# Kernel tuning notes

Measured on AMD Instinct MI355X. Metric: run time of the kernel, lower is better.

The kernel has to match this reference:

```python
import jax, jax.numpy as jnp
import numpy as np

NUM_EMBEDDINGS = 2048
EMBEDDING_DIM = 256
COMMITMENT_COST = 0.25


def setup_inputs() -> dict:
    key = jax.random.key(0)
    k1, k2 = jax.random.split(key)
    z_e = jax.random.normal(k1, (64, EMBEDDING_DIM, 32, 32), dtype=jnp.float32)
    # nn.Embedding weight initialized uniform(-1/K, 1/K)
    bound = 1.0 / NUM_EMBEDDINGS
    codebook = jax.random.uniform(k2, (NUM_EMBEDDINGS, EMBEDDING_DIM),
                                  dtype=jnp.float32, minval=-bound, maxval=bound)
    return {"z_e": z_e, "codebook": codebook}


def reference(z_e, codebook):
    B, C, H, W = z_e.shape  # C == embedding_dim
    K = codebook.shape[0]
    sg = jax.lax.stop_gradient

    # [B, C, H, W] -> [B*H*W, C]
    z_e_flat = jnp.transpose(z_e, (0, 2, 3, 1)).reshape(-1, C)

    # squared L2 distances: ||z||^2 - 2 z E^T + ||E||^2  -> [N, K]
    distances = (jnp.sum(z_e_flat ** 2, axis=1, keepdims=True)
                 - 2.0 * jnp.matmul(z_e_flat, codebook.T)
                 + jnp.sum(codebook ** 2, axis=1))
    indices = jnp.argmin(distances, axis=1)  # [N]

    encodings = jax.nn.one_hot(indices, K, dtype=z_e_flat.dtype)  # [N, K]
    z_q_flat = codebook[indices]  # [N, C] embedding gather
    z_q = jnp.transpose(z_q_flat.reshape(B, H, W, C), (0, 3, 1, 2))

    codebook_loss = jnp.mean((z_q_flat - sg(z_e_flat)) ** 2)
    commitment_loss = jnp.mean((sg(z_q_flat) - z_e_flat) ** 2)
    loss = codebook_loss + COMMITMENT_COST * commitment_loss

    e_mean = jnp.mean(encodings, axis=0)  # [K]
    perplexity = jnp.exp(-jnp.sum(e_mean * jnp.log(e_mean + 1e-10)))

    # straight-through estimator
    z_q_st = z_e + sg(z_q - z_e)
    return z_q_st, loss, perplexity, encodings
```

## Files before the change

### kernel.cpp

```cpp
#include <hip/hip_runtime.h>
#include <hip/hip_bf16.h>
#include <math.h>

#define NTOT 65536
#define KCB  2048
#define CDIM 256
#define HW   1024

#define OUT_LOSS 16777216
#define OUT_PERP 16777217
#define OUT_ENC  16777218

#define CBB_OFF_F 33554448

#define WS_CK   262144
#define WS_IDX  270336
#define WS_CNT  532480
#define WS_PART 540672

#define MARGIN 3e-3f
#define CAP 1024

typedef __attribute__((ext_vector_type(8))) short short8;
typedef __attribute__((ext_vector_type(4))) float f32x4;

__device__ inline unsigned enc_f(float x) {
    unsigned u = __float_as_uint(x);
    return (u & 0x80000000u) ? ~u : (u | 0x80000000u);
}
__device__ inline float dec_f(unsigned e) {
    unsigned u = (e & 0x80000000u) ? (e ^ 0x80000000u) : ~e;
    return __uint_as_float(u);
}

__device__ inline void lds_min_u64(unsigned long long* p, unsigned long long v) {
    unsigned long long old = *p;
    while (v < old) {
        unsigned long long assumed = old;
        old = atomicCAS(p, assumed, v);
        if (old == assumed) break;
    }
}

__global__ __launch_bounds__(256) void k_prep_cb(const float* __restrict__ cb, ushort* __restrict__ cbb,
                                                 float* __restrict__ ck, int* __restrict__ cntK) {
    const int tid = threadIdx.x;
    const int wv = tid >> 6, lane = tid & 63;
    const int r = blockIdx.x * 4 + wv;
    const float* row = cb + (size_t)r * CDIM;
    float4 v = *(const float4*)(row + lane * 4);
    ushort4 o;
    __hip_bfloat16 h;
    h = __float2bfloat16(v.x); o.x = *(ushort*)&h;
    h = __float2bfloat16(v.y); o.y = *(ushort*)&h;
    h = __float2bfloat16(v.z); o.z = *(ushort*)&h;
    h = __float2bfloat16(v.w); o.w = *(ushort*)&h;
    *(ushort4*)(cbb + (size_t)r * CDIM + lane * 4) = o;
    float s = v.x*v.x + v.y*v.y + v.z*v.z + v.w*v.w;
    for (int off = 32; off >= 1; off >>= 1) s += __shfl_down(s, off, 64);
    if (lane == 0) ck[r] = s;
    if (lane == 1) cntK[r] = 0;
}

__global__ __launch_bounds__(256, 2) void k_main(
    const float* __restrict__ z, const float* __restrict__ cb,
    const ushort* __restrict__ cbb, const float* __restrict__ ckg,
    int* __restrict__ indices, int* __restrict__ cntK,
    float* __restrict__ out0, double* __restrict__ part)
{
    __shared__ float ztb[CDIM * 65];
    __shared__ union {
        struct {
            unsigned long long wmin[4][64];
            float thrRow[64];
            float srowL[64];
            int   candRK[CAP];
        } p1;
        float  qc[32 * 65];
        double sh[256];
    } u;
    __shared__ unsigned long long best[64];
    __shared__ int cnt;
    __shared__ int allscan;

    const int tid = threadIdx.x;
    const int w = tid >> 6, lane = tid & 63;
    const int col = lane & 15, quad = lane >> 4;
    const int n0 = blockIdx.x * 64;
    const int b = n0 >> 10, hw0 = n0 & 1023;

    {
        const int hwq = tid & 15, csub = (tid >> 4) & 3;
#pragma unroll
        for (int i = 0; i < 16; ++i) {
            const int c = w * 64 + i * 4 + csub;
            float4 v = *(const float4*)(z + ((size_t)b * CDIM + c) * HW + hw0 + hwq * 4);
            float* dst = ztb + c * 65 + hwq * 4;
            dst[0] = v.x; dst[1] = v.y; dst[2] = v.z; dst[3] = v.w;
        }
    }
    if (tid == 0) { cnt = 0; allscan = 0; }
    __syncthreads();

    short8 areg[4][8];
#pragma unroll
    for (int nt = 0; nt < 4; ++nt)
#pragma unroll
        for (int cs = 0; cs < 8; ++cs) {
            short8 a;
#pragma unroll
            for (int j = 0; j < 8; ++j) {
                __hip_bfloat16 h = __float2bfloat16(ztb[(cs * 32 + quad * 8 + j) * 65 + nt * 16 + col]);
                a[j] = *(ushort*)&h;
            }
            areg[nt][cs] = a;
        }

    if (tid < 64) {
        float s = 0.f;
#pragma unroll 8
        for (int c = 0; c < CDIM; ++c) { float v = ztb[c * 65 + tid]; s = fmaf(v, v, s); }
        u.p1.srowL[tid] = s;
    }

    float m1[16], m2[16]; int k1[16];
#pragma unroll
    for (int s = 0; s < 16; ++s) { m1[s] = INFINITY; m2[s] = INFINITY; k1[s] = 0; }

    for (int k0 = 0; k0 < KCB; k0 += 128) {
        const int kb = k0 + w * 32;
#pragma unroll
        for (int kt = 0; kt < 2; ++kt) {
            const int kk = kb + kt * 16 + col;
            const ushort* bbase = cbb + (size_t)kk * CDIM + quad * 8;
            short8 bfrag[8];
#pragma unroll
            for (int cs = 0; cs < 8; ++cs) bfrag[cs] = *(const short8*)(bbase + cs * 32);
            f32x4 acc[4];
#pragma unroll
            for (int nt = 0; nt < 4; ++nt) acc[nt] = (f32x4){0.f, 0.f, 0.f, 0.f};
#pragma unroll
            for (int cs = 0; cs < 8; ++cs)
#pragma unroll
                for (int nt = 0; nt < 4; ++nt)
                    acc[nt] = __builtin_amdgcn_mfma_f32_16x16x32_bf16(areg[nt][cs], bfrag[cs], acc[nt], 0, 0, 0);
            const float ckv = ckg[kk];
#pragma unroll
            for (int nt = 0; nt < 4; ++nt)
#pragma unroll
                for (int r = 0; r < 4; ++r) {
                    float dt = fmaf(-2.0f, acc[nt][r], ckv);
                    const int s = nt * 4 + r;
                    bool c = dt < m1[s];
                    m2[s] = fminf(m2[s], fmaxf(dt, m1[s]));
                    m1[s] = fminf(m1[s], dt);
                    k1[s] = c ? kk : k1[s];
                }
        }
    }

#pragma unroll
    for (int s = 0; s < 16; ++s) {
        unsigned long long v = ((unsigned long long)enc_f(m1[s]) << 32) | (unsigned)k1[s];
#pragma unroll
        for (int m = 1; m <= 8; m <<= 1) {
            unsigned long long o = __shfl_xor(v, m, 64);
            v = (o < v) ? o : v;
        }
        if (col == 0) u.p1.wmin[w][(s >> 2) * 16 + quad * 4 + (s & 3)] = v;
    }
    if (tid < 64) best[tid] = ~0ull;
    __syncthreads();
    if (tid < 64) {
        unsigned long long v = u.p1.wmin[0][tid];
        unsigned long long o = u.p1.wmin[1][tid]; v = (o < v) ? o : v;
        o = u.p1.wmin[2][tid]; v = (o < v) ? o : v;
        o = u.p1.wmin[3][tid]; v = (o < v) ? o : v;
        u.p1.thrRow[tid] = dec_f((unsigned)(v >> 32)) + MARGIN;
    }
    __syncthreads();

#pragma unroll
    for (int s = 0; s < 16; ++s) {
        const int row = (s >> 2) * 16 + quad * 4 + (s & 3);
        const float thr = u.p1.thrRow[row];
        if (m1[s] <= thr) {
            int p = atomicAdd(&cnt, 1);
            if (p < CAP) u.p1.candRK[p] = (row << 16) | k1[s];
        }
        if (m2[s] <= thr) {
            int p = atomicAdd(&cnt, 32);
            if (p + 32 <= CAP) {
#pragma unroll
                for (int k0i = 0; k0i < 16; ++k0i) {
                    int kbase = k0i * 128 + w * 32 + col;
                    u.p1.candRK[p + 2 * k0i]     = (row << 16) | kbase;
                    u.p1.candRK[p + 2 * k0i + 1] = (row << 16) | (kbase + 16);
                }
            }
        }
    }
    __syncthreads();
    if (cnt > CAP) { if (tid == 0) allscan = 1; }
    __syncthreads();
    const int nc = allscan ? 0 : min(cnt, CAP);

    for (int t = tid; t < nc; t += 256) {
        const int rc = u.p1.candRK[t];
        const int row = rc >> 16, k = rc & 0xFFFF;
        const float* cp = cb + (size_t)k * CDIM;
        float m = 0.f;
#pragma unroll 8
        for (int c = 0; c < CDIM; ++c) m = fmaf(ztb[c * 65 + row], cp[c], m);
        float d = (u.p1.srowL[row] - 2.0f * m) + ckg[k];
        unsigned long long pk = ((unsigned long long)__float_as_uint(d) << 32) | (unsigned)k;
        lds_min_u64(&best[row], pk);
    }
    if (allscan) {
        for (int row = 0; row < 64; ++row) {
            const float sr = u.p1.srowL[row];
            for (int kq = 0; kq < 8; ++kq) {
                int k = kq * 256 + tid;
                const float* cp = cb + (size_t)k * CDIM;
                float m = 0.f;
#pragma unroll 8
                for (int c = 0; c < CDIM; ++c) m = fmaf(ztb[c * 65 + row], cp[c], m);
                float d = (sr - 2.0f * m) + ckg[k];
                unsigned long long pk = ((unsigned long long)__float_as_uint(d) << 32) | (unsigned)k;
                lds_min_u64(&best[row], pk);
            }
        }
    }
    __syncthreads();
    if (tid < 64) {
        int bk = (int)(best[tid] & 0xFFFFFFFFull);
        indices[n0 + tid] = bk;
        atomicAdd(&cntK[bk], 1);
    }

    const size_t ebase = ((size_t)b * CDIM) * HW + hw0 + lane;
    const int krow = (int)(best[lane] & 0xFFFFFFFFull);
    const float* crow = cb + (size_t)krow * CDIM;
    double acc = 0.0;
    for (int q = 0; q < 8; ++q) {
        {
            float4 v0 = *(const float4*)(crow + q * 32 + w * 8);
            float4 v1 = *(const float4*)(crow + q * 32 + w * 8 + 4);
            float* dst = u.qc + (w * 8) * 65 + lane;
            dst[0 * 65] = v0.x; dst[1 * 65] = v0.y; dst[2 * 65] = v0.z; dst[3 * 65] = v0.w;
            dst[4 * 65] = v1.x; dst[5 * 65] = v1.y; dst[6 * 65] = v1.z; dst[7 * 65] = v1.w;
        }
        __syncthreads();
        if (w == (q >> 1)) {
            const int j0 = (q & 1) * 32;
#pragma unroll 4
            for (int jj = 0; jj < 32; ++jj) {
                const int c = w * 64 + j0 + jj;
                float ze = ztb[c * 65 + lane];
                float qv = u.qc[jj * 65 + lane];
                float d = qv - ze;
                out0[ebase + ((size_t)c << 10)] = ze + d;
                acc += (double)d * (double)d;
            }
        }
        __syncthreads();
    }
    u.sh[tid] = acc;
    __syncthreads();
    for (int s2 = 128; s2 > 0; s2 >>= 1) {
        if (tid < s2) u.sh[tid] += u.sh[tid + s2];
        __syncthreads();
    }
    if (tid == 0) part[blockIdx.x] = u.sh[0];
}

__global__ __launch_bounds__(256) void k_encodings(const int* __restrict__ idx, float4* __restrict__ p4,
                                                   float* __restrict__ tail) {
    __shared__ int sidx[17];
    const int tid = threadIdx.x;
    const size_t g0 = (size_t)blockIdx.x * 8192;
    const long f0 = 4L * (long)g0 - 2;
    int nlo = (int)(f0 >> 11); if (nlo < 0) nlo = 0;
    if (tid < 17) { int n = nlo + tid; sidx[tid] = (n < NTOT) ? idx[n] : -1; }
    __syncthreads();
    const float4 zv = make_float4(0.f, 0.f, 0.f, 0.f);
    for (int i = 0; i < 32; ++i) {
        size_t g = g0 + (size_t)i * 256 + tid;
        long fe = 4L * (long)g - 2;
        float4 v = zv;
        if (fe < 0) {
            int kk = sidx[0];
            if (kk == 0) v.z = 1.f;
            if (kk == 1) v.w = 1.f;
        } else {
            int n = (int)(fe >> 11);
            int k0c = (int)(fe & 2047);
            if (k0c >= 2045) {
#pragma unroll
                for (int j = 0; j < 4; ++j) {
                    long fej = fe + j;
                    int nj = (int)(fej >> 11);
                    int kj = (int)(fej & 2047);
                    int li = nj - nlo;
                    int kk = (li >= 0 && li < 17) ? sidx[li] : -2;
                    ((float*)&v)[j] = (kk == kj) ? 1.f : 0.f;
                }
            } else {
                int d = sidx[n - nlo] - k0c;
                if (d >= 0 && d < 4) ((float*)&v)[d] = 1.f;
            }
        }
        p4[g] = v;
    }
    if (blockIdx.x == 0 && tid == 0) {
        int kk = idx[NTOT - 1];
        tail[0] = (kk == 2046) ? 1.f : 0.f;
        tail[1] = (kk == 2047) ? 1.f : 0.f;
    }
}

__global__ __launch_bounds__(256) void k_finalize(const double* __restrict__ part, const int* __restrict__ cnt,
                                                  float* __restrict__ out) {
    __shared__ double sh[256];
    double a = 0.0;
    for (int i = threadIdx.x; i < 1024; i += 256) a += part[i];
    sh[threadIdx.x] = a; __syncthreads();
    for (int s = 128; s > 0; s >>= 1) { if (threadIdx.x < s) sh[threadIdx.x] += sh[threadIdx.x + s]; __syncthreads(); }
    double total = sh[0];
    __syncthreads();
    double p = 0.0;
    for (int i = threadIdx.x; i < 2048; i += 256) {
        double pm = (double)cnt[i] / 65536.0;
        p += pm * log(pm + 1e-10);
    }
    sh[threadIdx.x] = p; __syncthreads();
    for (int s = 128; s > 0; s >>= 1) { if (threadIdx.x < s) sh[threadIdx.x] += sh[threadIdx.x + s]; __syncthreads(); }
    if (threadIdx.x == 0) {
        double mean = total / ((double)NTOT * (double)CDIM);
        out[OUT_LOSS] = (float)(mean * 1.25);
        out[OUT_PERP] = (float)exp(-sh[0]);
    }
}

extern "C" void kernel_launch(void* const* d_in, const int* in_sizes, int n_in,
                              void* d_out, int out_size, void* d_ws, size_t ws_size,
                              hipStream_t stream) {
    const float* z  = (const float*)d_in[0];
    const float* cb = (const float*)d_in[1];
    float* out = (float*)d_out;
    char* ws = (char*)d_ws;
    float*  ck   = (float*)(ws + WS_CK);
    int*    idx  = (int*)(ws + WS_IDX);
    int*    cnt  = (int*)(ws + WS_CNT);
    double* part = (double*)(ws + WS_PART);
    ushort* cbb = (ushort*)(out + CBB_OFF_F);

    hipLaunchKernelGGL(k_prep_cb,   dim3(512),  dim3(256), 0, stream, cb, cbb, ck, cnt);
    hipLaunchKernelGGL(k_main,      dim3(1024), dim3(256), 0, stream, z, cb, cbb, ck, idx, cnt, out, part);
    hipLaunchKernelGGL(k_encodings, dim3(4096), dim3(256), 0, stream, idx, (float4*)(out + OUT_LOSS),
                       out + (OUT_LOSS + (size_t)33554432 * 4));
    hipLaunchKernelGGL(k_finalize,  dim3(1),    dim3(256), 0, stream, part, cnt, out);
}
```

Measured before the change: 862.7 us.

## Fuse one-hot encodings write into main kernel, interleaved with distance MFMA loop

The separate k_encodings pass is removed. Each main block now zero-fills its 64-row slab of the encodings output inside the codebook loop and then scatters a 1.0 at the argmin index. The region of the output that doubles as scratch for the bf16 codebook is skipped during the main kernel. A merged tail kernel fills that region from the indices and also computes the loss and perplexity. This aims to overlap the 512 MB of encoding stores with MFMA compute and save a launch, at the cost of extra store traffic inside the compute loop and tricky aliasing logic.

Result: faster. 826.4 us (-4.2%).

```diff
diff --git a/kernel.cpp b/kernel.cpp
--- a/kernel.cpp
+++ b/kernel.cpp
@@ -12,6 +12,8 @@
 #define OUT_ENC  16777218
 
 #define CBB_OFF_F 33554448
+#define CBB_ABS_LO 33554448
+#define CBB_ABS_HI 34078736
 
 #define WS_CK   262144
 #define WS_IDX  270336
@@ -89,6 +91,10 @@
     const int n0 = blockIdx.x * 64;
     const int b = n0 >> 10, hw0 = n0 & 1023;
 
+    const int SB = OUT_ENC + n0 * 2048;
+    const int slabF4 = SB + 2;
+    const float4 zero4 = make_float4(0.f, 0.f, 0.f, 0.f);
+
     {
         const int hwq = tid & 15, csub = (tid >> 4) & 3;
 #pragma unroll
@@ -99,6 +105,13 @@
             dst[0] = v.x; dst[1] = v.y; dst[2] = v.z; dst[3] = v.w;
         }
     }
+    if (tid == 0) {
+        if (!(SB >= CBB_ABS_LO && SB < CBB_ABS_HI)) *(float2*)(out0 + SB) = make_float2(0.f, 0.f);
+    }
+    if (tid == 1) {
+        const int Ft = SB + 131070;
+        if (!(Ft >= CBB_ABS_LO && Ft < CBB_ABS_HI)) *(float2*)(out0 + Ft) = make_float2(0.f, 0.f);
+    }
     if (tid == 0) { cnt = 0; allscan = 0; }
     __syncthreads();
 
@@ -128,6 +141,16 @@
     for (int s = 0; s < 16; ++s) { m1[s] = INFINITY; m2[s] = INFINITY; k1[s] = 0; }
 
     for (int k0 = 0; k0 < KCB; k0 += 128) {
+        {
+            const int it0 = (k0 >> 7) * 8;
+#pragma unroll
+            for (int ii = 0; ii < 8; ++ii) {
+                const int j = (it0 + ii) * 256 + tid;
+                const int F = slabF4 + 4 * j;
+                if (j < 32767 && !(F >= CBB_ABS_LO && F < CBB_ABS_HI))
+                    *(float4*)(out0 + F) = zero4;
+            }
+        }
         const int kb = k0 + w * 32;
 #pragma unroll
         for (int kt = 0; kt < 2; ++kt) {
@@ -236,6 +259,8 @@
         int bk = (int)(best[tid] & 0xFFFFFFFFull);
         indices[n0 + tid] = bk;
         atomicAdd(&cntK[bk], 1);
+        const int F1 = OUT_ENC + (n0 + tid) * 2048 + bk;
+        if (!(F1 >= CBB_ABS_LO && F1 < CBB_ABS_HI)) out0[F1] = 1.0f;
     }
 
     const size_t ebase = ((size_t)b * CDIM) * HW + hw0 + lane;
@@ -274,53 +299,22 @@
     if (tid == 0) part[blockIdx.x] = u.sh[0];
 }
 
-__global__ __launch_bounds__(256) void k_encodings(const int* __restrict__ idx, float4* __restrict__ p4,
-                                                   float* __restrict__ tail) {
-    __shared__ int sidx[17];
-    const int tid = threadIdx.x;
-    const size_t g0 = (size_t)blockIdx.x * 8192;
-    const long f0 = 4L * (long)g0 - 2;
-    int nlo = (int)(f0 >> 11); if (nlo < 0) nlo = 0;
-    if (tid < 17) { int n = nlo + tid; sidx[tid] = (n < NTOT) ? idx[n] : -1; }
-    __syncthreads();
-    const float4 zv = make_float4(0.f, 0.f, 0.f, 0.f);
-    for (int i = 0; i < 32; ++i) {
-        size_t g = g0 + (size_t)i * 256 + tid;
-        long fe = 4L * (long)g - 2;
-        float4 v = zv;
-        if (fe < 0) {
-            int kk = sidx[0];
-            if (kk == 0) v.z = 1.f;
-            if (kk == 1) v.w = 1.f;
-        } else {
-            int n = (int)(fe >> 11);
-            int k0c = (int)(fe & 2047);
-            if (k0c >= 2045) {
-#pragma unroll
-                for (int j = 0; j < 4; ++j) {
-                    long fej = fe + j;
-                    int nj = (int)(fej >> 11);
-                    int kj = (int)(fej & 2047);
-                    int li = nj - nlo;
-                    int kk = (li >= 0 && li < 17) ? sidx[li] : -2;
-                    ((float*)&v)[j] = (kk == kj) ? 1.f : 0.f;
-                }
-            } else {
-                int d = sidx[n - nlo] - k0c;
-                if (d >= 0 && d < 4) ((float*)&v)[d] = 1.f;
-            }
-        }
-        p4[g] = v;
-    }
-    if (blockIdx.x == 0 && tid == 0) {
-        int kk = idx[NTOT - 1];
-        tail[0] = (kk == 2046) ? 1.f : 0.f;
-        tail[1] = (kk == 2047) ? 1.f : 0.f;
-    }
-}
-
-__global__ __launch_bounds__(256) void k_finalize(const double* __restrict__ part, const int* __restrict__ cnt,
-                                                  float* __restrict__ out) {
+__global__ __launch_bounds__(256) void k_tail(const int* __restrict__ idx, const double* __restrict__ part,
+                                              const int* __restrict__ cnt, float* __restrict__ out) {
+    if (blockIdx.x < 512) {
+        const int t = blockIdx.x * 256 + threadIdx.x;
+        const int F = CBB_ABS_LO + 4 * t;
+        const int rel = F - OUT_ENC;
+        float4 v;
+#pragma unroll
+        for (int j = 0; j < 4; ++j) {
+            const int fr = rel + j;
+            const int n = fr >> 11, k = fr & 2047;
+            ((float*)&v)[j] = (idx[n] == k) ? 1.f : 0.f;
+        }
+        *(float4*)(out + F) = v;
+        return;
+    }
     __shared__ double sh[256];
     double a = 0.0;
     for (int i = threadIdx.x; i < 1024; i += 256) a += part[i];
@@ -355,9 +349,7 @@
     double* part = (double*)(ws + WS_PART);
     ushort* cbb = (ushort*)(out + CBB_OFF_F);
 
-    hipLaunchKernelGGL(k_prep_cb,   dim3(512),  dim3(256), 0, stream, cb, cbb, ck, cnt);
-    hipLaunchKernelGGL(k_main,      dim3(1024), dim3(256), 0, stream, z, cb, cbb, ck, idx, cnt, out, part);
-    hipLaunchKernelGGL(k_encodings, dim3(4096), dim3(256), 0, stream, idx, (float4*)(out + OUT_LOSS),
-                       out + (OUT_LOSS + (size_t)33554432 * 4));
-    hipLaunchKernelGGL(k_finalize,  dim3(1),    dim3(256), 0, stream, part, cnt, out);
-}
+    hipLaunchKernelGGL(k_prep_cb, dim3(512),  dim3(256), 0, stream, cb, cbb, ck, cnt);
+    hipLaunchKernelGGL(k_main,    dim3(1024), dim3(256), 0, stream, z, cb, cbb, ck, idx, cnt, out, part);
+    hipLaunchKernelGGL(k_tail,    dim3(513),  dim3(256), 0, stream, idx, part, cnt, out);
+}
```
